# Optimization experiments

Hardware: AMD Instinct MI355X
Metric: run time of the kernel (lower is better)

## Reference

```python
import jax, jax.numpy as jnp
import numpy as np
import math

EPS = 1e-5
ANGLES = [0, 30, 45, 60, 90, 135]
SIGMA = 0.3
POOL = 7  # top-hat neighbourhood


def make_masks(H, W):
    # Soft Gaussian stripe masks, one per angle: [A, H, W]
    ys = np.linspace(-1.0, 1.0, H)
    xs = np.linspace(-1.0, 1.0, W)
    gy, gx = np.meshgrid(ys, xs, indexing='ij')
    ms = []
    for a in ANGLES:
        t = a * math.pi / 180.0
        perp = gx * (-math.sin(t)) + gy * math.cos(t)
        ms.append(np.exp(-0.5 * (perp / SIGMA) ** 2))
    return jnp.asarray(np.stack(ms, axis=0), dtype=jnp.float32)


def dwconv1d(x, w):
    # x: [B, C, L], w: [C, 1, K] depthwise, 'same' padding (odd K)
    return jax.lax.conv_general_dilated(
        x, w, window_strides=(1,), padding='SAME',
        feature_group_count=x.shape[1],
        dimension_numbers=('NCH', 'OIH', 'NCH'))


def bn(x, gamma, beta, axes, pshape):
    # Training-mode batch norm (biased variance, as in torch forward)
    mean = x.mean(axes, keepdims=True)
    var = x.var(axes, keepdims=True)
    return (x - mean) * jax.lax.rsqrt(var + EPS) * gamma.reshape(pshape) + beta.reshape(pshape)


def maxpool_same(x, k):
    # torch MaxPool2d(k, stride=1, padding=k//2): pad with -inf
    p = k // 2
    return jax.lax.reduce_window(
        x, -jnp.inf, jax.lax.max,
        window_dimensions=(1, 1, k, k), window_strides=(1, 1, 1, 1),
        padding=[(0, 0), (0, 0), (p, p), (p, p)])


def setup_inputs() -> dict:
    key = jax.random.key(0)
    ks = jax.random.split(key, 8)
    B, C, H, W = 128, 576, 28, 28
    K = 3
    x = jax.random.normal(ks[0], (B, C, H, W), dtype=jnp.float32)
    h_w = jax.random.normal(ks[1], (C, 1, K), dtype=jnp.float32) * 0.2
    v_w = jax.random.normal(ks[2], (C, 1, K), dtype=jnp.float32) * 0.2
    f_w = jax.random.normal(ks[3], (C,), dtype=jnp.float32) * 0.2  # 1x1 dw conv = per-channel scale
    h_g = jnp.ones((C,), jnp.float32); h_b = jnp.zeros((C,), jnp.float32)
    v_g = jnp.ones((C,), jnp.float32); v_b = jnp.zeros((C,), jnp.float32)
    f_g = jnp.ones((C,), jnp.float32); f_b = jnp.zeros((C,), jnp.float32)
    return {"x": x, "h_w": h_w, "h_g": h_g, "h_b": h_b,
            "v_w": v_w, "v_g": v_g, "v_b": v_b,
            "f_w": f_w, "f_g": f_g, "f_b": f_b}


def reference(x, h_w, h_g, h_b, v_w, v_g, v_b, f_w, f_g, f_b):
    B, C, H, W = x.shape
    # Horizontal stream: mean over W -> dw conv1d over H -> BN1d -> sigmoid -> [B,C,H,1]
    ph = x.mean(axis=-1)                                   # [B, C, H]
    A_h = jax.nn.sigmoid(bn(dwconv1d(ph, h_w), h_g, h_b, (0, 2), (1, C, 1)))[..., None]
    # Vertical stream: mean over H -> dw conv1d over W -> BN1d -> sigmoid -> [B,C,1,W]
    pv = x.mean(axis=-2)                                   # [B, C, W]
    A_v = jax.nn.sigmoid(bn(dwconv1d(pv, v_w), v_g, v_b, (0, 2), (1, C, 1)))[:, :, None, :]
    # Focal spot stream: white top-hat -> per-channel scale -> BN2d -> sigmoid
    spots = maxpool_same(x, POOL) - x                      # [B, C, H, W]
    A_f = jax.nn.sigmoid(bn(spots * f_w[None, :, None, None], f_g, f_b, (0, 2, 3), (1, C, 1, 1)))
    # Orientation bank: masked global means, sigmoid per angle, mean over angles
    masks = make_masks(H, W)                               # [A, H, W]
    resp = jnp.einsum('bchw,ahw->bca', x, masks) / (H * W) # [B, C, A]
    A_t = jax.nn.sigmoid(resp).mean(axis=-1)[:, :, None, None]
    return x * A_h * A_v * A_f * A_t
```

## Files before the change

### kernel.cpp

```cpp
#include <hip/hip_runtime.h>
#include <math.h>

#define B 128
#define C 576
#define H 28
#define W 28
#define HW 784
#define NPLANE (B * C)
#define RMROWS 34
#define LOG2E 1.4426950408889634f

typedef float nfloat4 __attribute__((ext_vector_type(4)));

__device__ __forceinline__ float sigm2(float z2) { return 1.f / (1.f + exp2f(-z2)); }

__device__ __forceinline__ float4 fmax4(float4 a, float4 b) {
    a.x = fmaxf(a.x, b.x); a.y = fmaxf(a.y, b.y);
    a.z = fmaxf(a.z, b.z); a.w = fmaxf(a.w, b.w);
    return a;
}

__device__ __forceinline__ float4 hmax13(float4 Mv, float4 Lv, float4 Rv) {
    float mm   = fmaxf(fmaxf(Mv.x, Mv.y), fmaxf(Mv.z, Mv.w));
    float l23  = fmaxf(Lv.z, Lv.w);
    float l123 = fmaxf(Lv.y, l23);
    float r01  = fmaxf(Rv.x, Rv.y);
    float r012 = fmaxf(r01, Rv.z);
    float4 o;
    o.x = fmaxf(l123, mm);
    o.y = fmaxf(l23, fmaxf(mm, Rv.x));
    o.z = fmaxf(Lv.w, fmaxf(mm, r01));
    o.w = fmaxf(mm, r012);
    return o;
}

__device__ __forceinline__ float dpp_sum64(float v) {
    int t;
    t = __builtin_amdgcn_update_dpp(0, __float_as_int(v), 0x111, 0xf, 0xf, true);  v += __int_as_float(t);
    t = __builtin_amdgcn_update_dpp(0, __float_as_int(v), 0x112, 0xf, 0xf, true);  v += __int_as_float(t);
    t = __builtin_amdgcn_update_dpp(0, __float_as_int(v), 0x114, 0xf, 0xf, true);  v += __int_as_float(t);
    t = __builtin_amdgcn_update_dpp(0, __float_as_int(v), 0x118, 0xf, 0xf, true);  v += __int_as_float(t);
    t = __builtin_amdgcn_update_dpp(0, __float_as_int(v), 0x142, 0xa, 0xf, false); v += __int_as_float(t);
    t = __builtin_amdgcn_update_dpp(0, __float_as_int(v), 0x143, 0xc, 0xf, false); v += __int_as_float(t);
    return v;
}

__device__ __forceinline__ void wave_lds_fence() {
    asm volatile("s_waitcnt lgkmcnt(0)" ::: "memory");
    __builtin_amdgcn_sched_barrier(0);
}

__global__ void k0_init(float* __restrict__ masks, float* __restrict__ acc) {
    int idx = blockIdx.x * 256 + threadIdx.x;
    if (idx < 6 * C) acc[idx] = 0.f;
    if (idx < 6 * HW) {
        int a = idx / HW;
        int p = idx - a * HW;
        int r = p / W;
        int col = p - r * W;
        const float degs[6] = {0.f, 30.f, 45.f, 60.f, 90.f, 135.f};
        float t = degs[a] * 0.017453292519943295f;
        float gy = -1.f + r * (2.f / 27.f);
        float gx = -1.f + col * (2.f / 27.f);
        float perp = gx * (-sinf(t)) + gy * cosf(t);
        float z = perp * (1.f / 0.3f);
        masks[idx] = expf(-0.5f * z * z);
    }
}

__global__ __launch_bounds__(256, 3) void k1_stats(
    const float* __restrict__ x,
    const float* __restrict__ h_w, const float* __restrict__ v_w,
    const float* __restrict__ f_w, const float* __restrict__ masks,
    float* __restrict__ yh, float* __restrict__ yv,
    float* __restrict__ at, float* __restrict__ acc)
{
    const int tid = threadIdx.x;
    const int wvi = __builtin_amdgcn_readfirstlane(tid >> 6);
    const int l   = tid & 63;
    const int plane = blockIdx.x * 4 + wvi;
    const int c = plane % C;
    const float* xp = x + (size_t)plane * HW;

    __shared__ __align__(16) float uA[4][RMROWS * W];
    __shared__ __align__(16) float cpA[4][196];
    __shared__ __align__(16) float rpA[4][196];
    float* rm  = uA[wvi];
    float* sxv = rm + 3 * W;
    float* cp  = cpA[wvi];
    float* rp  = rpA[wvi];

    const int r0 = l / 7;
    const int u  = l - r0 * 7;
    const int q  = u * 4;
    const int qL = u ? q - 4 : 0;
    const int qR = (u < 6) ? q + 4 : 24;
    const bool act = (l < 49);

    const float4* mkA[6] = {
        (const float4*)(masks),          (const float4*)(masks + HW),
        (const float4*)(masks + 2 * HW), (const float4*)(masks + 3 * HW),
        (const float4*)(masks + 4 * HW), (const float4*)(masks + 5 * HW)};

    float4 Mv[4];
    float fs = 0.f, fss = 0.f;

    {
        float o0=0.f,o1=0.f,o2=0.f,o3=0.f,o4=0.f,o5=0.f;
        if (act) {
            float4 mk[24];
            #pragma unroll
            for (int k = 0; k < 4; ++k) Mv[k] = ((const float4*)xp)[l + 49 * k];
            #pragma unroll
            for (int a = 0; a < 6; ++a) {
                #pragma unroll
                for (int k = 0; k < 4; ++k) mk[a * 4 + k] = mkA[a][l + 49 * k];
            }
            __builtin_amdgcn_sched_barrier(0);

            float4 ca = make_float4(0.f, 0.f, 0.f, 0.f);
            float rw[4];
            #pragma unroll
            for (int k = 0; k < 4; ++k) {
                const int unit = l + 49 * k;
                float4 v = Mv[k];
                ((float4*)sxv)[unit] = v;
                ca.x += v.x; ca.y += v.y; ca.z += v.z; ca.w += v.w;
                rw[k] = (v.x + v.y) + (v.z + v.w);
            }
            ((float4*)cp)[l] = ca;
            ((float4*)rp)[l] = make_float4(rw[0], rw[1], rw[2], rw[3]);

            #pragma unroll
            for (int k = 0; k < 4; ++k) {
                float4 v = Mv[k];
                float4 m;
                m = mk[k];      o0 += v.x*m.x + v.y*m.y + v.z*m.z + v.w*m.w;
                m = mk[4 + k];  o1 += v.x*m.x + v.y*m.y + v.z*m.z + v.w*m.w;
                m = mk[8 + k];  o2 += v.x*m.x + v.y*m.y + v.z*m.z + v.w*m.w;
                m = mk[12 + k]; o3 += v.x*m.x + v.y*m.y + v.z*m.z + v.w*m.w;
                m = mk[16 + k]; o4 += v.x*m.x + v.y*m.y + v.z*m.z + v.w*m.w;
                m = mk[20 + k]; o5 += v.x*m.x + v.y*m.y + v.z*m.z + v.w*m.w;
            }
        }
        o0 = dpp_sum64(o0); o1 = dpp_sum64(o1); o2 = dpp_sum64(o2);
        o3 = dpp_sum64(o3); o4 = dpp_sum64(o4); o5 = dpp_sum64(o5);
        if (l == 63) {
            const float s784 = LOG2E / (float)HW;
            float t = sigm2(o0 * s784) + sigm2(o1 * s784) + sigm2(o2 * s784)
                    + sigm2(o3 * s784) + sigm2(o4 * s784) + sigm2(o5 * s784);
            at[plane] = t * (1.f / 6.f);
        }
    }
    wave_lds_fence();

    if (act) {
        #pragma unroll
        for (int k = 0; k < 4; ++k) {
            const int r = r0 + 7 * k;
            const float* row = sxv + r * W;
            float4 Lv = *(const float4*)(row + qL);
            float4 Rv = *(const float4*)(row + qR);
            float4 hv = hmax13(Mv[k], Lv, Rv);
            *(float4*)(rm + (r + 3) * W + q) = hv;
            if (k == 0 && r0 == 0) {
                *(float4*)(rm + 0 * W + q) = hv;
                *(float4*)(rm + 1 * W + q) = hv;
                *(float4*)(rm + 2 * W + q) = hv;
            }
            if (k == 3 && r0 == 6) {
                *(float4*)(rm + 31 * W + q) = hv;
                *(float4*)(rm + 32 * W + q) = hv;
                *(float4*)(rm + 33 * W + q) = hv;
            }
        }
    }
    wave_lds_fence();

    if (act) {
        #pragma unroll
        for (int k = 0; k < 4; ++k) {
            const int r = r0 + 7 * k;
            const float* vb = rm + r * W + q;
            float4 m = *(const float4*)vb;
            m = fmax4(m, *(const float4*)(vb + W));
            m = fmax4(m, *(const float4*)(vb + 2 * W));
            m = fmax4(m, *(const float4*)(vb + 3 * W));
            m = fmax4(m, *(const float4*)(vb + 4 * W));
            m = fmax4(m, *(const float4*)(vb + 5 * W));
            m = fmax4(m, *(const float4*)(vb + 6 * W));
            float s0 = m.x - Mv[k].x;
            float s1 = m.y - Mv[k].y;
            float s2 = m.z - Mv[k].z;
            float s3 = m.w - Mv[k].w;
            fs  += (s0 + s1) + (s2 + s3);
            fss += (s0 * s0 + s1 * s1) + (s2 * s2 + s3 * s3);
        }
    }

    float ph_r = 0.f;
    float4 pvv = make_float4(0.f, 0.f, 0.f, 0.f);
    if (l < 28) {
        const int rr = l % 7, kk = l / 7;
        const float* rb = rp + rr * 28 + kk;
        float s = ((rb[0] + rb[4]) + (rb[8] + rb[12]))
                + ((rb[16] + rb[20]) + rb[24]);
        ph_r = s * (1.f / 28.f);
    }
    if (l < 7) {
        const float4* cb = (const float4*)cp;
        float4 a = cb[l];
        #pragma unroll
        for (int j = 1; j < 7; ++j) {
            float4 b = cb[l + 7 * j];
            a.x += b.x; a.y += b.y; a.z += b.z; a.w += b.w;
        }
        pvv.x = a.x * (1.f / 28.f); pvv.y = a.y * (1.f / 28.f);
        pvv.z = a.z * (1.f / 28.f); pvv.w = a.w * (1.f / 28.f);
    }

    const float hw0 = h_w[c * 3], hw1 = h_w[c * 3 + 1], hw2 = h_w[c * 3 + 2];
    float yhv = 0.f;
    {
        float pm = __shfl_up(ph_r, 1);
        float pp = __shfl_down(ph_r, 1);
        if (l < 28) {
            float a = (l > 0) ? pm : 0.f;
            float d = (l < 27) ? pp : 0.f;
            yhv = hw0 * a + hw1 * ph_r + hw2 * d;
            yh[(size_t)plane * H + l] = yhv;
        }
    }
    const float vw0 = v_w[c * 3], vw1 = v_w[c * 3 + 1], vw2 = v_w[c * 3 + 2];
    float yvs = 0.f, yvq = 0.f;
    {
        float lf = __shfl_up(pvv.w, 1);
        float rg = __shfl_down(pvv.x, 1);
        if (l < 7) {
            float a0 = (l > 0) ? lf : 0.f;
            float d3 = (l < 6) ? rg : 0.f;
            float4 y;
            y.x = vw0 * a0    + vw1 * pvv.x + vw2 * pvv.y;
            y.y = vw0 * pvv.x + vw1 * pvv.y + vw2 * pvv.z;
            y.z = vw0 * pvv.y + vw1 * pvv.z + vw2 * pvv.w;
            y.w = vw0 * pvv.z + vw1 * pvv.w + vw2 * d3;
            ((float4*)(yv + (size_t)plane * W))[l] = y;
            yvs = (y.x + y.y) + (y.z + y.w);
            yvq = (y.x * y.x + y.y * y.y) + (y.z * y.z + y.w * y.w);
        }
    }
    float yhq = yhv * yhv;

    fs = dpp_sum64(fs);  fss = dpp_sum64(fss);
    yhv = dpp_sum64(yhv); yhq = dpp_sum64(yhq);
    yvs = dpp_sum64(yvs); yvq = dpp_sum64(yvq);

    if (l == 63) {
        const float fwc = f_w[c];
        atomicAdd(&acc[0 * C + c], yhv);
        atomicAdd(&acc[1 * C + c], yhq);
        atomicAdd(&acc[2 * C + c], yvs);
        atomicAdd(&acc[3 * C + c], yvq);
        atomicAdd(&acc[4 * C + c], fs * fwc);
        atomicAdd(&acc[5 * C + c], fss * fwc * fwc);
    }
}

__global__ __launch_bounds__(64) void k2_params(
    const float* __restrict__ acc, const float* __restrict__ f_w,
    const float* __restrict__ hg, const float* __restrict__ hb,
    const float* __restrict__ vg, const float* __restrict__ vb,
    const float* __restrict__ fg, const float* __restrict__ fb,
    float* __restrict__ params)
{
    int c = blockIdx.x * 64 + threadIdx.x;
    if (c >= C) return;
    const float inv_nh = 1.f / (float)(B * H);
    const float inv_nf = 1.f / (float)(B * HW);
    float m, v, sc;
    m = acc[c] * inv_nh;
    v = acc[C + c] * inv_nh - m * m;
    sc = hg[c] * rsqrtf(v + 1e-5f);
    params[c * 8 + 0] = sc * LOG2E; params[c * 8 + 1] = (hb[c] - m * sc) * LOG2E;

    m = acc[2 * C + c] * inv_nh;
    v = acc[3 * C + c] * inv_nh - m * m;
    sc = vg[c] * rsqrtf(v + 1e-5f);
    params[c * 8 + 2] = sc * LOG2E; params[c * 8 + 3] = (vb[c] - m * sc) * LOG2E;

    m = acc[4 * C + c] * inv_nf;
    v = acc[5 * C + c] * inv_nf - m * m;
    sc = fg[c] * rsqrtf(v + 1e-5f);
    params[c * 8 + 4] = sc * f_w[c] * LOG2E;
    params[c * 8 + 5] = (fb[c] - m * sc) * LOG2E;
}

__global__ __launch_bounds__(256, 8) void k3_apply(
    const float* __restrict__ x,
    const float* __restrict__ yh, const float* __restrict__ yv,
    const float* __restrict__ at, const float* __restrict__ params,
    float* __restrict__ out)
{
    const int tid = threadIdx.x;
    const int wvi = __builtin_amdgcn_readfirstlane(tid >> 6);
    const int l   = tid & 63;
    const int plane = blockIdx.x * 4 + wvi;
    const int c = plane % C;
    const float* xp = x + (size_t)plane * HW;

    __shared__ __align__(16) float uA[4][RMROWS * W];
    float* rm  = uA[wvi];
    float* sxv = rm + 3 * W;

    const int r0 = l / 7;
    const int u  = l - r0 * 7;
    const int q  = u * 4;
    const int qL = u ? q - 4 : 0;
    const int qR = (u < 6) ? q + 4 : 24;
    const bool act = (l < 49);

    const float4 pA = *(const float4*)(params + c * 8);
    const float2 pB = *(const float2*)(params + c * 8 + 4);
    const float atv = at[plane];

    float4 Mv[4];

    if (act) {
        #pragma unroll
        for (int k = 0; k < 4; ++k) {
            const int unit = l + 49 * k;
            Mv[k] = ((const float4*)xp)[unit];
            ((float4*)sxv)[unit] = Mv[k];
        }
    }
    wave_lds_fence();

    if (act) {
        #pragma unroll
        for (int k = 0; k < 4; ++k) {
            const int r = r0 + 7 * k;
            const float* row = sxv + r * W;
            float4 Lv = *(const float4*)(row + qL);
            float4 Rv = *(const float4*)(row + qR);
            float4 hv = hmax13(Mv[k], Lv, Rv);
            *(float4*)(rm + (r + 3) * W + q) = hv;
            if (k == 0 && r0 == 0) {
                *(float4*)(rm + 0 * W + q) = hv;
                *(float4*)(rm + 1 * W + q) = hv;
                *(float4*)(rm + 2 * W + q) = hv;
            }
            if (k == 3 && r0 == 6) {
                *(float4*)(rm + 31 * W + q) = hv;
                *(float4*)(rm + 32 * W + q) = hv;
                *(float4*)(rm + 33 * W + q) = hv;
            }
        }
    }
    wave_lds_fence();

    if (act) {
        float4 yv4 = ((const float4*)(yv + (size_t)plane * W))[u];
        float4 av;
        av.x = sigm2(pA.z * yv4.x + pA.w);
        av.y = sigm2(pA.z * yv4.y + pA.w);
        av.z = sigm2(pA.z * yv4.z + pA.w);
        av.w = sigm2(pA.z * yv4.w + pA.w);
        nfloat4* op = (nfloat4*)(out + (size_t)plane * HW);
        #pragma unroll
        for (int k = 0; k < 4; ++k) {
            const int r = r0 + 7 * k;
            const float* vb = rm + r * W + q;
            float4 m = *(const float4*)vb;
            m = fmax4(m, *(const float4*)(vb + W));
            m = fmax4(m, *(const float4*)(vb + 2 * W));
            m = fmax4(m, *(const float4*)(vb + 3 * W));
            m = fmax4(m, *(const float4*)(vb + 4 * W));
            m = fmax4(m, *(const float4*)(vb + 5 * W));
            m = fmax4(m, *(const float4*)(vb + 6 * W));
            float ahk = sigm2(pA.x * yh[(size_t)plane * H + r] + pA.y) * atv;
            nfloat4 o;
            o.x = Mv[k].x * ahk * av.x * sigm2(fmaf(pB.x, m.x, fmaf(-pB.x, Mv[k].x, pB.y)));
            o.y = Mv[k].y * ahk * av.y * sigm2(fmaf(pB.x, m.y, fmaf(-pB.x, Mv[k].y, pB.y)));
            o.z = Mv[k].z * ahk * av.z * sigm2(fmaf(pB.x, m.z, fmaf(-pB.x, Mv[k].z, pB.y)));
            o.w = Mv[k].w * ahk * av.w * sigm2(fmaf(pB.x, m.w, fmaf(-pB.x, Mv[k].w, pB.y)));
            __builtin_nontemporal_store(o, &op[l + 49 * k]);
        }
    }
}

extern "C" void kernel_launch(void* const* d_in, const int* in_sizes, int n_in,
                              void* d_out, int out_size, void* d_ws, size_t ws_size,
                              hipStream_t stream) {
    const float* x   = (const float*)d_in[0];
    const float* h_w = (const float*)d_in[1];
    const float* h_g = (const float*)d_in[2];
    const float* h_b = (const float*)d_in[3];
    const float* v_w = (const float*)d_in[4];
    const float* v_g = (const float*)d_in[5];
    const float* v_b = (const float*)d_in[6];
    const float* f_w = (const float*)d_in[7];
    const float* f_g = (const float*)d_in[8];
    const float* f_b = (const float*)d_in[9];
    float* out = (float*)d_out;
    float* ws = (float*)d_ws;

    float* masks  = ws;
    float* acc    = ws + 4704;
    float* params = ws + 8160;
    float* at     = ws + 12768;
    float* yh     = ws + 86496;
    float* yv     = ws + 2150880;

    k0_init<<<19, 256, 0, stream>>>(masks, acc);
    k1_stats<<<NPLANE / 4, 256, 0, stream>>>(x, h_w, v_w, f_w, masks, yh, yv, at, acc);
    k2_params<<<9, 64, 0, stream>>>(acc, f_w, h_g, h_b, v_g, v_b, f_g, f_b, params);
    k3_apply<<<NPLANE / 4, 256, 0, stream>>>(x, yh, yv, at, params, out);
}
```

Measured before the change: 207.7 us.

## Stage bf16 orientation masks in LDS per block and raise occupancy of stats kernel

```diff
diff --git a/kernel.cpp b/kernel.cpp
--- a/kernel.cpp
+++ b/kernel.cpp
@@ -50,7 +50,7 @@
     __builtin_amdgcn_sched_barrier(0);
 }
 
-__global__ void k0_init(float* __restrict__ masks, float* __restrict__ acc) {
+__global__ void k0_init(unsigned short* __restrict__ masks16, float* __restrict__ acc) {
     int idx = blockIdx.x * 256 + threadIdx.x;
     if (idx < 6 * C) acc[idx] = 0.f;
     if (idx < 6 * HW) {
@@ -64,14 +64,17 @@
         float gx = -1.f + col * (2.f / 27.f);
         float perp = gx * (-sinf(t)) + gy * cosf(t);
         float z = perp * (1.f / 0.3f);
-        masks[idx] = expf(-0.5f * z * z);
-    }
-}
-
-__global__ __launch_bounds__(256, 3) void k1_stats(
+        float m = expf(-0.5f * z * z);
+        unsigned int u = __float_as_uint(m);
+        unsigned int rnd = (u + 0x7fffu + ((u >> 16) & 1u)) >> 16;
+        masks16[idx] = (unsigned short)rnd;
+    }
+}
+
+__global__ __launch_bounds__(256, 5) void k1_stats(
     const float* __restrict__ x,
     const float* __restrict__ h_w, const float* __restrict__ v_w,
-    const float* __restrict__ f_w, const float* __restrict__ masks,
+    const float* __restrict__ f_w, const unsigned short* __restrict__ masks16,
     float* __restrict__ yh, float* __restrict__ yv,
     float* __restrict__ at, float* __restrict__ acc)
 {
@@ -85,6 +88,7 @@
     __shared__ __align__(16) float uA[4][RMROWS * W];
     __shared__ __align__(16) float cpA[4][196];
     __shared__ __align__(16) float rpA[4][196];
+    __shared__ __align__(16) unsigned short mlds[6 * HW];
     float* rm  = uA[wvi];
     float* sxv = rm + 3 * W;
     float* cp  = cpA[wvi];
@@ -97,29 +101,31 @@
     const int qR = (u < 6) ? q + 4 : 24;
     const bool act = (l < 49);
 
-    const float4* mkA[6] = {
-        (const float4*)(masks),          (const float4*)(masks + HW),
-        (const float4*)(masks + 2 * HW), (const float4*)(masks + 3 * HW),
-        (const float4*)(masks + 4 * HW), (const float4*)(masks + 5 * HW)};
-
     float4 Mv[4];
     float fs = 0.f, fss = 0.f;
+
+    if (act) {
+        #pragma unroll
+        for (int k = 0; k < 4; ++k) Mv[k] = ((const float4*)xp)[l + 49 * k];
+    }
+
+    {
+        const uint4* gm = (const uint4*)masks16;
+        uint4* lm = (uint4*)mlds;
+        #pragma unroll
+        for (int i = 0; i < 3; ++i) {
+            int j = tid + i * 256;
+            if (j < 588) lm[j] = gm[j];
+        }
+    }
+    __syncthreads();
 
     {
         float o0=0.f,o1=0.f,o2=0.f,o3=0.f,o4=0.f,o5=0.f;
         if (act) {
-            float4 mk[24];
-            #pragma unroll
-            for (int k = 0; k < 4; ++k) Mv[k] = ((const float4*)xp)[l + 49 * k];
-            #pragma unroll
-            for (int a = 0; a < 6; ++a) {
-                #pragma unroll
-                for (int k = 0; k < 4; ++k) mk[a * 4 + k] = mkA[a][l + 49 * k];
-            }
-            __builtin_amdgcn_sched_barrier(0);
-
             float4 ca = make_float4(0.f, 0.f, 0.f, 0.f);
             float rw[4];
+            const uint2* mp = (const uint2*)mlds;
             #pragma unroll
             for (int k = 0; k < 4; ++k) {
                 const int unit = l + 49 * k;
@@ -127,21 +133,21 @@
                 ((float4*)sxv)[unit] = v;
                 ca.x += v.x; ca.y += v.y; ca.z += v.z; ca.w += v.w;
                 rw[k] = (v.x + v.y) + (v.z + v.w);
+                #pragma unroll
+                for (int a = 0; a < 6; ++a) {
+                    uint2 d = mp[a * 196 + unit];
+                    float m0 = __uint_as_float(d.x << 16);
+                    float m1 = __uint_as_float(d.x & 0xffff0000u);
+                    float m2 = __uint_as_float(d.y << 16);
+                    float m3 = __uint_as_float(d.y & 0xffff0000u);
+                    float dot = v.x * m0 + v.y * m1 + v.z * m2 + v.w * m3;
+                    if (a == 0) o0 += dot; else if (a == 1) o1 += dot;
+                    else if (a == 2) o2 += dot; else if (a == 3) o3 += dot;
+                    else if (a == 4) o4 += dot; else o5 += dot;
+                }
             }
             ((float4*)cp)[l] = ca;
             ((float4*)rp)[l] = make_float4(rw[0], rw[1], rw[2], rw[3]);
-
-            #pragma unroll
-            for (int k = 0; k < 4; ++k) {
-                float4 v = Mv[k];
-                float4 m;
-                m = mk[k];      o0 += v.x*m.x + v.y*m.y + v.z*m.z + v.w*m.w;
-                m = mk[4 + k];  o1 += v.x*m.x + v.y*m.y + v.z*m.z + v.w*m.w;
-                m = mk[8 + k];  o2 += v.x*m.x + v.y*m.y + v.z*m.z + v.w*m.w;
-                m = mk[12 + k]; o3 += v.x*m.x + v.y*m.y + v.z*m.z + v.w*m.w;
-                m = mk[16 + k]; o4 += v.x*m.x + v.y*m.y + v.z*m.z + v.w*m.w;
-                m = mk[20 + k]; o5 += v.x*m.x + v.y*m.y + v.z*m.z + v.w*m.w;
-            }
         }
         o0 = dpp_sum64(o0); o1 = dpp_sum64(o1); o2 = dpp_sum64(o2);
         o3 = dpp_sum64(o3); o4 = dpp_sum64(o4); o5 = dpp_sum64(o5);
@@ -404,15 +410,15 @@
     float* out = (float*)d_out;
     float* ws = (float*)d_ws;
 
-    float* masks  = ws;
-    float* acc    = ws + 4704;
-    float* params = ws + 8160;
-    float* at     = ws + 12768;
-    float* yh     = ws + 86496;
-    float* yv     = ws + 2150880;
-
-    k0_init<<<19, 256, 0, stream>>>(masks, acc);
-    k1_stats<<<NPLANE / 4, 256, 0, stream>>>(x, h_w, v_w, f_w, masks, yh, yv, at, acc);
+    unsigned short* masks16 = (unsigned short*)ws;
+    float* acc    = ws + 2352;
+    float* params = ws + 5808;
+    float* at     = ws + 10416;
+    float* yh     = ws + 84144;
+    float* yv     = ws + 2148528;
+
+    k0_init<<<19, 256, 0, stream>>>(masks16, acc);
+    k1_stats<<<NPLANE / 4, 256, 0, stream>>>(x, h_w, v_w, f_w, masks16, yh, yv, at, acc);
     k2_params<<<9, 64, 0, stream>>>(acc, f_w, h_g, h_b, v_g, v_b, f_g, f_b, params);
     k3_apply<<<NPLANE / 4, 256, 0, stream>>>(x, yh, yv, at, params, out);
 }
```

Measured after the change: 230.7 us. +11.1%, slower.
